# Kernel tuning notes

Hardware: AMD Instinct MI355X
Metric: run time of the kernel (lower is better)

The kernel has to match this reference:

```python
import jax, jax.numpy as jnp
import numpy as np

N = 4096  # output_size
B = 4096  # batch rows
NEG_SLOPE = 0.02


def setup_inputs() -> dict:
    key = jax.random.key(0)
    k1, k2, k3, k4 = jax.random.split(key, 4)
    x = jax.random.normal(k1, (B, N), dtype=jnp.float32)
    W = jax.random.normal(k2, (N, N), dtype=jnp.float32)        # self.weights
    beta = jax.random.normal(k3, (1,), dtype=jnp.float32)       # self.beta (scalar param)
    beta_res = jax.random.normal(k4, (N,), dtype=jnp.float32)   # self.res.beta
    return {"x": x, "W": W, "beta": beta, "beta_res": beta_res}


def reference(x, W, beta, beta_res):
    # wrho = x.unsqueeze(1) * W.expand(B,-1,-1); row_sum = wrho.sum(2)  ==  x @ W.T
    row_sum = jnp.einsum("bj,ij->bi", x, W)                 # [B, N]
    out = jax.nn.relu(1.0 - beta + row_sum)                 # hlogic(1 - beta + row_sum)
    # ResEventually: relu(1 - (beta_res - (x + out))), then LeakyReLU(0.02)
    res = jax.nn.relu(1.0 - (beta_res - (x + out)))
    return jnp.where(res >= 0, res, NEG_SLOPE * res)
```

## Files before the change

kernel.cpp:

```cpp
#include <hip/hip_runtime.h>


#define NDIM 4096

typedef __bf16 bf16x8 __attribute__((ext_vector_type(8)));
typedef float f32x4 __attribute__((ext_vector_type(4)));

__device__ unsigned short f2bf(float f) {
    unsigned int x;
    __builtin_memcpy(&x, &f, 4);
    unsigned int r = x + 0x7FFFu + ((x >> 16) & 1u);
    return (unsigned short)(r >> 16);
}

__device__ unsigned int pack_bf2(float lo, float hi) {
    return (unsigned int)f2bf(lo) | ((unsigned int)f2bf(hi) << 16);
}

__device__ inline void gload16(const uint4* g, unsigned int* l) {
    __builtin_amdgcn_global_load_lds(
        (const __attribute__((address_space(1))) unsigned int*)g,
        (__attribute__((address_space(3))) unsigned int*)l,
        16, 0, 0);
}

__global__ void convert_f32_bf16_kernel(const float* src, unsigned int* dst) {
    const size_t i = ((size_t)blockIdx.x * blockDim.x + threadIdx.x) * 8;
    float4 v0 = *(const float4*)(src + i);
    float4 v1 = *(const float4*)(src + i + 4);
    uint4 u;
    u.x = pack_bf2(v0.x, v0.y);
    u.y = pack_bf2(v0.z, v0.w);
    u.z = pack_bf2(v1.x, v1.y);
    u.w = pack_bf2(v1.z, v1.w);
    *(uint4*)(dst + i / 2) = u;
}

__global__ void ResFCEventuallyLayer_82205674045459_kernel(
    const unsigned int* Xbf, const unsigned int* Wbf,
    const float* X, const float* Bp, const float* Br,
    float* out)
{
    __shared__ __align__(16) unsigned int sA[128 * 16];
    __shared__ __align__(16) unsigned int sB[128 * 16];

    const int t    = threadIdx.x;
    const int lane = t & 63;
    const int wave = t >> 6;
    const int quad = lane >> 4;
    const int l16  = lane & 15;
    const int wm   = wave >> 1;
    const int wn   = wave & 1;

    const int bm0 = blockIdx.y * 128;
    const int bn0 = blockIdx.x * 128;

    const int c0 = t, c1 = t + 256;
    const uint4* gA0 = (const uint4*)Xbf + (size_t)(bm0 + (c0 >> 2)) * 512 + (c0 & 3);
    const uint4* gA1 = (const uint4*)Xbf + (size_t)(bm0 + (c1 >> 2)) * 512 + (c1 & 3);
    const uint4* gB0 = (const uint4*)Wbf + (size_t)(bn0 + (c0 >> 2)) * 512 + (c0 & 3);
    const uint4* gB1 = (const uint4*)Wbf + (size_t)(bn0 + (c1 >> 2)) * 512 + (c1 & 3);

    unsigned int* lA0 = sA + wave * 256;
    unsigned int* lA1 = sA + wave * 256 + 1024;
    unsigned int* lB0 = sB + wave * 256;
    unsigned int* lB1 = sB + wave * 256 + 1024;

    const bf16x8* pa = (const bf16x8*)sA + (wm * 64 + l16) * 4 + quad;
    const bf16x8* pb = (const bf16x8*)sB + (wn * 64 + l16) * 4 + quad;

    f32x4 acc[4][4];
    for (int i = 0; i < 4; i++)
        for (int j = 0; j < 4; j++)
            for (int r = 0; r < 4; r++)
                acc[i][j][r] = 0.0f;

    for (int s = 0; s < NDIM / 32; s++) {
        __syncthreads();
        gload16(gA0 + (size_t)s * 4, lA0);
        gload16(gA1 + (size_t)s * 4, lA1);
        gload16(gB0 + (size_t)s * 4, lB0);
        gload16(gB1 + (size_t)s * 4, lB1);
        __syncthreads();

        bf16x8 af[4], bfr[4];
        for (int mt = 0; mt < 4; mt++) af[mt]  = pa[mt * 64];
        for (int nt = 0; nt < 4; nt++) bfr[nt] = pb[nt * 64];

        for (int mt = 0; mt < 4; mt++)
            for (int nt = 0; nt < 4; nt++)
                acc[mt][nt] = __builtin_amdgcn_mfma_f32_16x16x32_bf16(
                    af[mt], bfr[nt], acc[mt][nt], 0, 0, 0);
    }

    const float one_m_beta = 1.0f - Bp[0];
    for (int nt = 0; nt < 4; nt++) {
        const int n = bn0 + wn * 64 + nt * 16 + l16;
        const float br = Br[n];
        for (int mt = 0; mt < 4; mt++) {
            const int mbase = bm0 + wm * 64 + mt * 16 + quad * 4;
            for (int r = 0; r < 4; r++) {
                const size_t idx = (size_t)(mbase + r) * NDIM + n;
                float v = acc[mt][nt][r] + one_m_beta;
                if (v < 0.0f) v = 0.0f;
                float res = 1.0f - br + X[idx] + v;
                if (res < 0.0f) res = 0.0f;
                out[idx] = res;
            }
        }
    }
}

__global__ void resfc_fallback_kernel(
    const float* X, const float* W,
    const float* Bp, const float* Br,
    float* out)
{
    __shared__ __align__(16) unsigned int sA[128 * 16];
    __shared__ __align__(16) unsigned int sB[128 * 16];

    const int t    = threadIdx.x;
    const int lane = t & 63;
    const int wave = t >> 6;
    const int quad = lane >> 4;
    const int l16  = lane & 15;
    const int wm   = wave >> 1;
    const int wn   = wave & 1;

    const int bm0 = blockIdx.y * 128;
    const int bn0 = blockIdx.x * 128;

    const float* gA[4];
    const float* gB[4];
    int ldsIdx[4];
    for (int c = 0; c < 4; c++) {
        const int ch   = t + c * 256;
        const int row  = ch >> 3;
        const int col4 = ch & 7;
        gA[c] = X + (size_t)(bm0 + row) * NDIM + col4 * 4;
        gB[c] = W + (size_t)(bn0 + row) * NDIM + col4 * 4;
        ldsIdx[c] = row * 16 + col4 * 2;
    }

    const bf16x8* pa = (const bf16x8*)sA + (wm * 64 + l16) * 4 + quad;
    const bf16x8* pb = (const bf16x8*)sB + (wn * 64 + l16) * 4 + quad;

    f32x4 acc[4][4];
    for (int i = 0; i < 4; i++)
        for (int j = 0; j < 4; j++)
            for (int r = 0; r < 4; r++)
                acc[i][j][r] = 0.0f;

    for (int k0 = 0; k0 < NDIM; k0 += 32) {
        float4 va[4], vb[4];
        for (int c = 0; c < 4; c++) {
            va[c] = *(const float4*)(gA[c] + k0);
            vb[c] = *(const float4*)(gB[c] + k0);
        }
        __syncthreads();
        for (int c = 0; c < 4; c++) {
            uint2 ua, ub;
            ua.x = pack_bf2(va[c].x, va[c].y);
            ua.y = pack_bf2(va[c].z, va[c].w);
            ub.x = pack_bf2(vb[c].x, vb[c].y);
            ub.y = pack_bf2(vb[c].z, vb[c].w);
            *(uint2*)(sA + ldsIdx[c]) = ua;
            *(uint2*)(sB + ldsIdx[c]) = ub;
        }
        __syncthreads();

        bf16x8 af[4], bfr[4];
        for (int mt = 0; mt < 4; mt++) af[mt]  = pa[mt * 64];
        for (int nt = 0; nt < 4; nt++) bfr[nt] = pb[nt * 64];

        for (int mt = 0; mt < 4; mt++)
            for (int nt = 0; nt < 4; nt++)
                acc[mt][nt] = __builtin_amdgcn_mfma_f32_16x16x32_bf16(
                    af[mt], bfr[nt], acc[mt][nt], 0, 0, 0);
    }

    const float one_m_beta = 1.0f - Bp[0];
    for (int nt = 0; nt < 4; nt++) {
        const int n = bn0 + wn * 64 + nt * 16 + l16;
        const float br = Br[n];
        for (int mt = 0; mt < 4; mt++) {
            const int mbase = bm0 + wm * 64 + mt * 16 + quad * 4;
            for (int r = 0; r < 4; r++) {
                const size_t idx = (size_t)(mbase + r) * NDIM + n;
                float v = acc[mt][nt][r] + one_m_beta;
                if (v < 0.0f) v = 0.0f;
                float res = 1.0f - br + X[idx] + v;
                if (res < 0.0f) res = 0.0f;
                out[idx] = res;
            }
        }
    }
}

extern "C" void kernel_launch(void* const* d_in, const int* in_sizes, int n_in,
                              void* d_out, int out_size, void* d_ws, size_t ws_size,
                              hipStream_t stream) {
    (void)in_sizes; (void)n_in; (void)out_size;

    const float* X  = (const float*)d_in[0];
    const float* W  = (const float*)d_in[1];
    const float* Bp = (const float*)d_in[2];
    const float* Br = (const float*)d_in[3];
    float* out      = (float*)d_out;

    const size_t elems   = (size_t)NDIM * NDIM;
    const size_t bf_need = elems * 2 * 2;

    dim3 gemm_grid(NDIM / 128, NDIM / 128);
    dim3 block(256);

    if (ws_size >= bf_need) {
        unsigned int* Xbf = (unsigned int*)d_ws;
        unsigned int* Wbf = (unsigned int*)d_ws + elems / 2;

        dim3 cvt_grid((unsigned int)(elems / 8 / 256));
        hipLaunchKernelGGL(convert_f32_bf16_kernel, cvt_grid, block, 0, stream, X, Xbf);
        hipLaunchKernelGGL(convert_f32_bf16_kernel, cvt_grid, block, 0, stream, W, Wbf);
        hipLaunchKernelGGL(ResFCEventuallyLayer_82205674045459_kernel,
                           gemm_grid, block, 0, stream, Xbf, Wbf, X, Bp, Br, out);
    } else {
        hipLaunchKernelGGL(resfc_fallback_kernel,
                           gemm_grid, block, 0, stream, X, W, Bp, Br, out);
    }
}
```

Baseline: 344.1 us.

## Rewrite bf16 GEMM with 256x256 tiles, double-buffered LDS pipeline, and swizzle

The main GEMM kernel moves from 128x128 tiles with 256 threads and a single-buffered K=32 loop to 256x256 tiles with 512 threads. It now uses a K=64 step, double-buffered LDS fed by async global-to-LDS loads, and an interleaved barrier and priority schedule that overlaps loads with MFMA. It also XOR-swizzles the LDS layout to avoid bank conflicts and remaps block ids so neighbouring blocks share rows and columns in cache. The goal is to hide memory latency and raise data reuse, at the cost of heavy register pressure (128 accumulator floats per thread) and fragile hand-tuned waitcnt and barrier ordering.

```diff
diff --git a/kernel.cpp b/kernel.cpp
--- a/kernel.cpp
+++ b/kernel.cpp
@@ -36,69 +36,163 @@
     *(uint4*)(dst + i / 2) = u;
 }
 
-__global__ void ResFCEventuallyLayer_82205674045459_kernel(
+#define BAR()   __builtin_amdgcn_s_barrier()
+#define LGKM0() do { asm volatile("s_waitcnt lgkmcnt(0)" ::: "memory"); \
+                     __builtin_amdgcn_sched_barrier(0); } while (0)
+#define VMCNT(n) asm volatile("s_waitcnt vmcnt(" #n ")" ::: "memory")
+#define PRIO(x) __builtin_amdgcn_s_setprio(x)
+
+#define STAGE_A(buf, h, S) do { \
+    gload16(Ab4 + (offA[2*(h)]   + (S)*8), &sAU[buf][(2*(h))*2048   + wq]); \
+    gload16(Ab4 + (offA[2*(h)+1] + (S)*8), &sAU[buf][(2*(h)+1)*2048 + wq]); \
+} while (0)
+#define STAGE_B(buf, h, S) do { \
+    gload16(Bb4 + (offB[2*(h)]   + (S)*8), &sBU[buf][(2*(h))*2048   + wq]); \
+    gload16(Bb4 + (offB[2*(h)+1] + (S)*8), &sBU[buf][(2*(h)+1)*2048 + wq]); \
+} while (0)
+
+#define READ_A4(dst, pbuf, mt0) do { \
+    _Pragma("unroll") for (int _m = 0; _m < 4; _m++) { \
+        dst[_m][0] = (pbuf)[afB + ((mt0) + _m) * 128]; \
+        dst[_m][1] = (pbuf)[afB + ((mt0) + _m) * 128 + 64]; } \
+} while (0)
+#define READ_B2(dst, pbuf, nt0) do { \
+    _Pragma("unroll") for (int _n = 0; _n < 2; _n++) { \
+        dst[_n][0] = (pbuf)[bfB + ((nt0) + _n) * 128]; \
+        dst[_n][1] = (pbuf)[bfB + ((nt0) + _n) * 128 + 64]; } \
+} while (0)
+
+#define MM16(afr, bfr, mt0, nt0) do { \
+    _Pragma("unroll") for (int _m = 0; _m < 4; _m++) \
+    _Pragma("unroll") for (int _n = 0; _n < 2; _n++) { \
+        acc[(mt0)+_m][(nt0)+_n] = __builtin_amdgcn_mfma_f32_16x16x32_bf16( \
+            afr[_m][0], bfr[_n][0], acc[(mt0)+_m][(nt0)+_n], 0, 0, 0); \
+        acc[(mt0)+_m][(nt0)+_n] = __builtin_amdgcn_mfma_f32_16x16x32_bf16( \
+            afr[_m][1], bfr[_n][1], acc[(mt0)+_m][(nt0)+_n], 0, 0, 0); } \
+} while (0)
+
+__global__ void __launch_bounds__(512, 2)
+ResFCEventuallyLayer_82205674045459_kernel(
     const unsigned int* Xbf, const unsigned int* Wbf,
     const float* X, const float* Bp, const float* Br,
     float* out)
 {
-    __shared__ __align__(16) unsigned int sA[128 * 16];
-    __shared__ __align__(16) unsigned int sB[128 * 16];
+    __shared__ __align__(16) unsigned int sAU[2][8192];
+    __shared__ __align__(16) unsigned int sBU[2][8192];
 
     const int t    = threadIdx.x;
     const int lane = t & 63;
     const int wave = t >> 6;
     const int quad = lane >> 4;
     const int l16  = lane & 15;
-    const int wm   = wave >> 1;
-    const int wn   = wave & 1;
-
-    const int bm0 = blockIdx.y * 128;
-    const int bn0 = blockIdx.x * 128;
-
-    const int c0 = t, c1 = t + 256;
-    const uint4* gA0 = (const uint4*)Xbf + (size_t)(bm0 + (c0 >> 2)) * 512 + (c0 & 3);
-    const uint4* gA1 = (const uint4*)Xbf + (size_t)(bm0 + (c1 >> 2)) * 512 + (c1 & 3);
-    const uint4* gB0 = (const uint4*)Wbf + (size_t)(bn0 + (c0 >> 2)) * 512 + (c0 & 3);
-    const uint4* gB1 = (const uint4*)Wbf + (size_t)(bn0 + (c1 >> 2)) * 512 + (c1 & 3);
-
-    unsigned int* lA0 = sA + wave * 256;
-    unsigned int* lA1 = sA + wave * 256 + 1024;
-    unsigned int* lB0 = sB + wave * 256;
-    unsigned int* lB1 = sB + wave * 256 + 1024;
-
-    const bf16x8* pa = (const bf16x8*)sA + (wm * 64 + l16) * 4 + quad;
-    const bf16x8* pb = (const bf16x8*)sB + (wn * 64 + l16) * 4 + quad;
-
-    f32x4 acc[4][4];
-    for (int i = 0; i < 4; i++)
+    const int wm   = wave >> 2;
+    const int wn   = wave & 3;
+    const int wq   = wave * 256;
+
+    const int bid = blockIdx.x;
+    const int swz = ((bid & 7) << 5) | (bid >> 3);
+    const int bm0 = (swz >> 4) * 256;
+    const int bn0 = (swz & 15) * 256;
+
+    const uint4* Ab4 = (const uint4*)Xbf;
+    const uint4* Bb4 = (const uint4*)Wbf;
+
+    int offA[4], offB[4];
+#pragma unroll
+    for (int rr = 0; rr < 4; rr++) {
+        const int p   = rr * 512 + t;
+        const int r   = (p >> 2) & 15;
+        const int sub = p >> 6;
+        const int sr  = sub >> 1, sc = sub & 1;
+        const int c8  = (p & 3) ^ (((r >> 3) & 1) << 1);
+        const int row = sr * 16 + r;
+        const int gc  = sc * 4 + c8;
+        offA[rr] = (bm0 + row) * 512 + gc;
+        offB[rr] = (bn0 + row) * 512 + gc;
+    }
+
+    const int laneByte = l16 * 64 + ((quad * 16) ^ (((l16 >> 3) & 1) << 5));
+    const int afB = (wm * 16384 + laneByte) >> 4;
+    const int bfB = (wn * 8192  + laneByte) >> 4;
+
+    const bf16x8* pA0 = (const bf16x8*)sAU[0];
+    const bf16x8* pA1 = (const bf16x8*)sAU[1];
+    const bf16x8* pB0 = (const bf16x8*)sBU[0];
+    const bf16x8* pB1 = (const bf16x8*)sBU[1];
+
+    f32x4 acc[8][4];
+#pragma unroll
+    for (int i = 0; i < 8; i++)
+#pragma unroll
         for (int j = 0; j < 4; j++)
+#pragma unroll
             for (int r = 0; r < 4; r++)
                 acc[i][j][r] = 0.0f;
 
-    for (int s = 0; s < NDIM / 32; s++) {
-        __syncthreads();
-        gload16(gA0 + (size_t)s * 4, lA0);
-        gload16(gA1 + (size_t)s * 4, lA1);
-        gload16(gB0 + (size_t)s * 4, lB0);
-        gload16(gB1 + (size_t)s * 4, lB1);
-        __syncthreads();
-
-        bf16x8 af[4], bfr[4];
-        for (int mt = 0; mt < 4; mt++) af[mt]  = pa[mt * 64];
-        for (int nt = 0; nt < 4; nt++) bfr[nt] = pb[nt * 64];
-
-        for (int mt = 0; mt < 4; mt++)
-            for (int nt = 0; nt < 4; nt++)
-                acc[mt][nt] = __builtin_amdgcn_mfma_f32_16x16x32_bf16(
-                    af[mt], bfr[nt], acc[mt][nt], 0, 0, 0);
+    bf16x8 af0[4][2], af1[4][2], bf0[2][2], bf1[2][2];
+
+    STAGE_A(0, 0, 0); STAGE_B(0, 0, 0); STAGE_B(0, 1, 0); STAGE_A(0, 1, 0);
+    STAGE_A(1, 0, 1); STAGE_B(1, 0, 1); STAGE_B(1, 1, 1);
+    VMCNT(6);
+    BAR();
+
+    for (int j = 0; j < 32; j++) {
+        const int S1 = 2 * j + 1;
+        const int S2 = (2 * j + 2) & 63;
+        const int S3 = (2 * j + 3) & 63;
+
+        READ_A4(af0, pA0, 0); READ_B2(bf0, pB0, 0);
+        STAGE_A(1, 1, S1);
+        BAR(); LGKM0();
+        PRIO(1); MM16(af0, bf0, 0, 0); PRIO(0);
+        BAR();
+        READ_B2(bf1, pB0, 2);
+        BAR(); LGKM0();
+        PRIO(1); MM16(af0, bf1, 0, 2); PRIO(0);
+        BAR();
+        READ_A4(af1, pA0, 4);
+        STAGE_B(0, 0, S2);
+        BAR(); LGKM0();
+        PRIO(1); MM16(af1, bf1, 4, 2); PRIO(0);
+        BAR();
+        STAGE_B(0, 1, S2);
+        STAGE_A(0, 0, S2);
+        BAR();
+        PRIO(1); MM16(af1, bf0, 4, 0); PRIO(0);
+        VMCNT(6);
+        BAR();
+
+        READ_A4(af0, pA1, 0); READ_B2(bf0, pB1, 0);
+        STAGE_A(0, 1, S2);
+        BAR(); LGKM0();
+        PRIO(1); MM16(af0, bf0, 0, 0); PRIO(0);
+        BAR();
+        READ_B2(bf1, pB1, 2);
+        BAR(); LGKM0();
+        PRIO(1); MM16(af0, bf1, 0, 2); PRIO(0);
+        BAR();
+        READ_A4(af1, pA1, 4);
+        STAGE_B(1, 0, S3);
+        BAR(); LGKM0();
+        PRIO(1); MM16(af1, bf1, 4, 2); PRIO(0);
+        BAR();
+        STAGE_B(1, 1, S3);
+        STAGE_A(1, 0, S3);
+        BAR();
+        PRIO(1); MM16(af1, bf0, 4, 0); PRIO(0);
+        VMCNT(6);
+        BAR();
     }
 
     const float one_m_beta = 1.0f - Bp[0];
+#pragma unroll
     for (int nt = 0; nt < 4; nt++) {
         const int n = bn0 + wn * 64 + nt * 16 + l16;
         const float br = Br[n];
-        for (int mt = 0; mt < 4; mt++) {
-            const int mbase = bm0 + wm * 64 + mt * 16 + quad * 4;
+#pragma unroll
+        for (int mt = 0; mt < 8; mt++) {
+            const int mbase = bm0 + wm * 128 + mt * 16 + quad * 4;
+#pragma unroll
             for (int r = 0; r < 4; r++) {
                 const size_t idx = (size_t)(mbase + r) * NDIM + n;
                 float v = acc[mt][nt][r] + one_m_beta;
@@ -211,7 +305,6 @@
     const size_t elems   = (size_t)NDIM * NDIM;
     const size_t bf_need = elems * 2 * 2;
 
-    dim3 gemm_grid(NDIM / 128, NDIM / 128);
     dim3 block(256);
 
     if (ws_size >= bf_need) {
@@ -222,9 +315,10 @@
         hipLaunchKernelGGL(convert_f32_bf16_kernel, cvt_grid, block, 0, stream, X, Xbf);
         hipLaunchKernelGGL(convert_f32_bf16_kernel, cvt_grid, block, 0, stream, W, Wbf);
         hipLaunchKernelGGL(ResFCEventuallyLayer_82205674045459_kernel,
-                           gemm_grid, block, 0, stream, Xbf, Wbf, X, Bp, Br, out);
+                           dim3(256), dim3(512), 0, stream, Xbf, Wbf, X, Bp, Br, out);
     } else {
         hipLaunchKernelGGL(resfc_fallback_kernel,
-                           gemm_grid, block, 0, stream, X, W, Bp, Br, out);
-    }
-}
+                           dim3(NDIM / 128, NDIM / 128), block, 0, stream,
+                           X, W, Bp, Br, out);
+    }
+}
```

Result: faster. 323.0 us (-6.1%).

## Double-buffer LDS, enlarge GEMM tile to 256x128, swizzle LDS and blocks

Applied to the files above, without the earlier changes.

The bf16 GEMM kernel moves from a 128x128 tile with a single LDS buffer and two barriers per k-step to a 256x128 tile with double-buffered LDS. The next k-slice is issued via global_load_lds while the current one is computed. An XOR swizzle on the LDS layout is meant to cut bank conflicts, and a block-index swizzle groups blocks for L2 reuse. The two conversion kernels are merged into one launch. Each wave now holds twice as many accumulators (8x4 MFMA tiles), which raises register pressure, and launch_bounds(256,2) limits occupancy.

```diff
diff --git a/kernel.cpp b/kernel.cpp
--- a/kernel.cpp
+++ b/kernel.cpp
@@ -24,8 +24,14 @@
         16, 0, 0);
 }
 
-__global__ void convert_f32_bf16_kernel(const float* src, unsigned int* dst) {
-    const size_t i = ((size_t)blockIdx.x * blockDim.x + threadIdx.x) * 8;
+__global__ void convert_f32_bf16_kernel(const float* X, unsigned int* Xbf,
+                                        const float* W, unsigned int* Wbf) {
+    unsigned int bid = blockIdx.x;
+    const float* src;
+    unsigned int* dst;
+    if (bid < 8192) { src = X; dst = Xbf; }
+    else            { src = W; dst = Wbf; bid -= 8192; }
+    const size_t i = ((size_t)bid * blockDim.x + threadIdx.x) * 8;
     float4 v0 = *(const float4*)(src + i);
     float4 v1 = *(const float4*)(src + i + 4);
     uint4 u;
@@ -36,13 +42,35 @@
     *(uint4*)(dst + i / 2) = u;
 }
 
-__global__ void ResFCEventuallyLayer_82205674045459_kernel(
+#define STAGE(buf, S) do { \
+    gload16(Ab4 + offA[0] + (S) * 4, &sAU[buf][0 * 1024 + wq]); \
+    gload16(Ab4 + offA[1] + (S) * 4, &sAU[buf][1 * 1024 + wq]); \
+    gload16(Ab4 + offA[2] + (S) * 4, &sAU[buf][2 * 1024 + wq]); \
+    gload16(Ab4 + offA[3] + (S) * 4, &sAU[buf][3 * 1024 + wq]); \
+    gload16(Bb4 + offB[0] + (S) * 4, &sBU[buf][0 * 1024 + wq]); \
+    gload16(Bb4 + offB[1] + (S) * 4, &sBU[buf][1 * 1024 + wq]); \
+} while (0)
+
+#define COMPUTE(b) do { \
+    bf16x8 af[8], bfr[4]; \
+    _Pragma("unroll") for (int _m = 0; _m < 8; _m++) \
+        af[_m] = ((const bf16x8*)sAU[b])[afB + _m * 64]; \
+    _Pragma("unroll") for (int _n = 0; _n < 4; _n++) \
+        bfr[_n] = ((const bf16x8*)sBU[b])[bfB + _n * 64]; \
+    _Pragma("unroll") for (int _m = 0; _m < 8; _m++) \
+    _Pragma("unroll") for (int _n = 0; _n < 4; _n++) \
+        acc[_m][_n] = __builtin_amdgcn_mfma_f32_16x16x32_bf16( \
+            af[_m], bfr[_n], acc[_m][_n], 0, 0, 0); \
+} while (0)
+
+__global__ void __launch_bounds__(256, 2)
+ResFCEventuallyLayer_82205674045459_kernel(
     const unsigned int* Xbf, const unsigned int* Wbf,
     const float* X, const float* Bp, const float* Br,
     float* out)
 {
-    __shared__ __align__(16) unsigned int sA[128 * 16];
-    __shared__ __align__(16) unsigned int sB[128 * 16];
+    __shared__ __align__(16) unsigned int sAU[2][4096];
+    __shared__ __align__(16) unsigned int sBU[2][2048];
 
     const int t    = threadIdx.x;
     const int lane = t & 63;
@@ -51,20 +79,106 @@
     const int l16  = lane & 15;
     const int wm   = wave >> 1;
     const int wn   = wave & 1;
+    const int wq   = wave * 256;
+
+    const int bid = blockIdx.x;
+    const int swz = ((bid & 7) << 6) | (bid >> 3);
+    const int bm0 = (swz >> 5) * 256;
+    const int bn0 = (swz & 31) * 128;
+
+    const uint4* Ab4 = (const uint4*)Xbf;
+    const uint4* Bb4 = (const uint4*)Wbf;
+
+    int offA[4], offB[2];
+#pragma unroll
+    for (int rr = 0; rr < 4; rr++) {
+        const int p  = rr * 256 + t;
+        const int cl = (p & 3) ^ ((((p >> 2) & 15) >> 3) << 1);
+        offA[rr] = (bm0 + (p >> 2)) * 512 + cl;
+    }
+#pragma unroll
+    for (int rr = 0; rr < 2; rr++) {
+        const int p  = rr * 256 + t;
+        const int cl = (p & 3) ^ ((((p >> 2) & 15) >> 3) << 1);
+        offB[rr] = (bn0 + (p >> 2)) * 512 + cl;
+    }
+
+    const int laneByte = l16 * 64 + ((quad * 16) ^ (((l16 >> 3) & 1) << 5));
+    const int afB = (wm * 8192 + laneByte) >> 4;
+    const int bfB = (wn * 4096 + laneByte) >> 4;
+
+    f32x4 acc[8][4];
+#pragma unroll
+    for (int i = 0; i < 8; i++)
+#pragma unroll
+        for (int j = 0; j < 4; j++)
+#pragma unroll
+            for (int r = 0; r < 4; r++)
+                acc[i][j][r] = 0.0f;
+
+    STAGE(0, 0);
+    __syncthreads();
+
+    for (int s = 0; s < 128; s += 2) {
+        STAGE(1, s + 1);
+        COMPUTE(0);
+        __syncthreads();
+        STAGE(0, (s + 2) & 127);
+        COMPUTE(1);
+        __syncthreads();
+    }
+
+    const float one_m_beta = 1.0f - Bp[0];
+#pragma unroll
+    for (int nt = 0; nt < 4; nt++) {
+        const int n = bn0 + wn * 64 + nt * 16 + l16;
+        const float br = Br[n];
+#pragma unroll
+        for (int mt = 0; mt < 8; mt++) {
+            const int mbase = bm0 + wm * 128 + mt * 16 + quad * 4;
+#pragma unroll
+            for (int r = 0; r < 4; r++) {
+                const size_t idx = (size_t)(mbase + r) * NDIM + n;
+                float v = acc[mt][nt][r] + one_m_beta;
+                if (v < 0.0f) v = 0.0f;
+                float res = 1.0f - br + X[idx] + v;
+                if (res < 0.0f) res = 0.0f;
+                out[idx] = res;
+            }
+        }
+    }
+}
+
+__global__ void resfc_fallback_kernel(
+    const float* X, const float* W,
+    const float* Bp, const float* Br,
+    float* out)
+{
+    __shared__ __align__(16) unsigned int sA[128 * 16];
+    __shared__ __align__(16) unsigned int sB[128 * 16];
+
+    const int t    = threadIdx.x;
+    const int lane = t & 63;
+    const int wave = t >> 6;
+    const int quad = lane >> 4;
+    const int l16  = lane & 15;
+    const int wm   = wave >> 1;
+    const int wn   = wave & 1;
 
     const int bm0 = blockIdx.y * 128;
     const int bn0 = blockIdx.x * 128;
 
-    const int c0 = t, c1 = t + 256;
-    const uint4* gA0 = (const uint4*)Xbf + (size_t)(bm0 + (c0 >> 2)) * 512 + (c0 & 3);
-    const uint4* gA1 = (const uint4*)Xbf + (size_t)(bm0 + (c1 >> 2)) * 512 + (c1 & 3);
-    const uint4* gB0 = (const uint4*)Wbf + (size_t)(bn0 + (c0 >> 2)) * 512 + (c0 & 3);
-    const uint4* gB1 = (const uint4*)Wbf + (size_t)(bn0 + (c1 >> 2)) * 512 + (c1 & 3);
-
-    unsigned int* lA0 = sA + wave * 256;
-    unsigned int* lA1 = sA + wave * 256 + 1024;
-    unsigned int* lB0 = sB + wave * 256;
-    unsigned int* lB1 = sB + wave * 256 + 1024;
+    const float* gA[4];
+    const float* gB[4];
+    int ldsIdx[4];
+    for (int c = 0; c < 4; c++) {
+        const int ch   = t + c * 256;
+        const int row  = ch >> 3;
+        const int col4 = ch & 7;
+        gA[c] = X + (size_t)(bm0 + row) * NDIM + col4 * 4;
+        gB[c] = W + (size_t)(bn0 + row) * NDIM + col4 * 4;
+        ldsIdx[c] = row * 16 + col4 * 2;
+    }
 
     const bf16x8* pa = (const bf16x8*)sA + (wm * 64 + l16) * 4 + quad;
     const bf16x8* pb = (const bf16x8*)sB + (wn * 64 + l16) * 4 + quad;
@@ -75,12 +189,22 @@
             for (int r = 0; r < 4; r++)
                 acc[i][j][r] = 0.0f;
 
-    for (int s = 0; s < NDIM / 32; s++) {
-        __syncthreads();
-        gload16(gA0 + (size_t)s * 4, lA0);
-        gload16(gA1 + (size_t)s * 4, lA1);
-        gload16(gB0 + (size_t)s * 4, lB0);
-        gload16(gB1 + (size_t)s * 4, lB1);
+    for (int k0 = 0; k0 < NDIM; k0 += 32) {
+        float4 va[4], vb[4];
+        for (int c = 0; c < 4; c++) {
+            va[c] = *(const float4*)(gA[c] + k0);
+            vb[c] = *(const float4*)(gB[c] + k0);
+        }
+        __syncthreads();
+        for (int c = 0; c < 4; c++) {
+            uint2 ua, ub;
+            ua.x = pack_bf2(va[c].x, va[c].y);
+            ua.y = pack_bf2(va[c].z, va[c].w);
+            ub.x = pack_bf2(vb[c].x, vb[c].y);
+            ub.y = pack_bf2(vb[c].z, vb[c].w);
+            *(uint2*)(sA + ldsIdx[c]) = ua;
+            *(uint2*)(sB + ldsIdx[c]) = ub;
+        }
         __syncthreads();
 
         bf16x8 af[4], bfr[4];
@@ -111,92 +235,6 @@
     }
 }
 
-__global__ void resfc_fallback_kernel(
-    const float* X, const float* W,
-    const float* Bp, const float* Br,
-    float* out)
-{
-    __shared__ __align__(16) unsigned int sA[128 * 16];
-    __shared__ __align__(16) unsigned int sB[128 * 16];
-
-    const int t    = threadIdx.x;
-    const int lane = t & 63;
-    const int wave = t >> 6;
-    const int quad = lane >> 4;
-    const int l16  = lane & 15;
-    const int wm   = wave >> 1;
-    const int wn   = wave & 1;
-
-    const int bm0 = blockIdx.y * 128;
-    const int bn0 = blockIdx.x * 128;
-
-    const float* gA[4];
-    const float* gB[4];
-    int ldsIdx[4];
-    for (int c = 0; c < 4; c++) {
-        const int ch   = t + c * 256;
-        const int row  = ch >> 3;
-        const int col4 = ch & 7;
-        gA[c] = X + (size_t)(bm0 + row) * NDIM + col4 * 4;
-        gB[c] = W + (size_t)(bn0 + row) * NDIM + col4 * 4;
-        ldsIdx[c] = row * 16 + col4 * 2;
-    }
-
-    const bf16x8* pa = (const bf16x8*)sA + (wm * 64 + l16) * 4 + quad;
-    const bf16x8* pb = (const bf16x8*)sB + (wn * 64 + l16) * 4 + quad;
-
-    f32x4 acc[4][4];
-    for (int i = 0; i < 4; i++)
-        for (int j = 0; j < 4; j++)
-            for (int r = 0; r < 4; r++)
-                acc[i][j][r] = 0.0f;
-
-    for (int k0 = 0; k0 < NDIM; k0 += 32) {
-        float4 va[4], vb[4];
-        for (int c = 0; c < 4; c++) {
-            va[c] = *(const float4*)(gA[c] + k0);
-            vb[c] = *(const float4*)(gB[c] + k0);
-        }
-        __syncthreads();
-        for (int c = 0; c < 4; c++) {
-            uint2 ua, ub;
-            ua.x = pack_bf2(va[c].x, va[c].y);
-            ua.y = pack_bf2(va[c].z, va[c].w);
-            ub.x = pack_bf2(vb[c].x, vb[c].y);
-            ub.y = pack_bf2(vb[c].z, vb[c].w);
-            *(uint2*)(sA + ldsIdx[c]) = ua;
-            *(uint2*)(sB + ldsIdx[c]) = ub;
-        }
-        __syncthreads();
-
-        bf16x8 af[4], bfr[4];
-        for (int mt = 0; mt < 4; mt++) af[mt]  = pa[mt * 64];
-        for (int nt = 0; nt < 4; nt++) bfr[nt] = pb[nt * 64];
-
-        for (int mt = 0; mt < 4; mt++)
-            for (int nt = 0; nt < 4; nt++)
-                acc[mt][nt] = __builtin_amdgcn_mfma_f32_16x16x32_bf16(
-                    af[mt], bfr[nt], acc[mt][nt], 0, 0, 0);
-    }
-
-    const float one_m_beta = 1.0f - Bp[0];
-    for (int nt = 0; nt < 4; nt++) {
-        const int n = bn0 + wn * 64 + nt * 16 + l16;
-        const float br = Br[n];
-        for (int mt = 0; mt < 4; mt++) {
-            const int mbase = bm0 + wm * 64 + mt * 16 + quad * 4;
-            for (int r = 0; r < 4; r++) {
-                const size_t idx = (size_t)(mbase + r) * NDIM + n;
-                float v = acc[mt][nt][r] + one_m_beta;
-                if (v < 0.0f) v = 0.0f;
-                float res = 1.0f - br + X[idx] + v;
-                if (res < 0.0f) res = 0.0f;
-                out[idx] = res;
-            }
-        }
-    }
-}
-
 extern "C" void kernel_launch(void* const* d_in, const int* in_sizes, int n_in,
                               void* d_out, int out_size, void* d_ws, size_t ws_size,
                               hipStream_t stream) {
@@ -211,20 +249,17 @@
     const size_t elems   = (size_t)NDIM * NDIM;
     const size_t bf_need = elems * 2 * 2;
 
-    dim3 gemm_grid(NDIM / 128, NDIM / 128);
-    dim3 block(256);
-
     if (ws_size >= bf_need) {
         unsigned int* Xbf = (unsigned int*)d_ws;
         unsigned int* Wbf = (unsigned int*)d_ws + elems / 2;
 
-        dim3 cvt_grid((unsigned int)(elems / 8 / 256));
-        hipLaunchKernelGGL(convert_f32_bf16_kernel, cvt_grid, block, 0, stream, X, Xbf);
-        hipLaunchKernelGGL(convert_f32_bf16_kernel, cvt_grid, block, 0, stream, W, Wbf);
+        hipLaunchKernelGGL(convert_f32_bf16_kernel, dim3(16384), dim3(256),
+                           0, stream, X, Xbf, W, Wbf);
         hipLaunchKernelGGL(ResFCEventuallyLayer_82205674045459_kernel,
-                           gemm_grid, block, 0, stream, Xbf, Wbf, X, Bp, Br, out);
+                           dim3(512), dim3(256), 0, stream, Xbf, Wbf, X, Bp, Br, out);
     } else {
         hipLaunchKernelGGL(resfc_fallback_kernel,
-                           gemm_grid, block, 0, stream, X, W, Bp, Br, out);
-    }
-}
+                           dim3(NDIM / 128, NDIM / 128), dim3(256), 0, stream,
+                           X, W, Bp, Br, out);
+    }
+}
```

Result: slower. 351.4 us (+2.1%).
